# Performance work log

Measured on AMD Instinct MI355X. Metric: run time of the kernel, lower is better.

The kernel has to match this reference:

```python
import jax, jax.numpy as jnp
import numpy as np

NUM_CHUNKS = 8
TOP_K = 2
IN_FEATURES = 4096
OUT_FEATURES = 4096
BATCH = 16384
CHUNK_IN = IN_FEATURES // NUM_CHUNKS
CHUNK_OUT = OUT_FEATURES // NUM_CHUNKS


def setup_inputs() -> dict:
    key = jax.random.key(0)
    kx, kw, kb = jax.random.split(key, 3)
    x = jax.random.normal(kx, (BATCH, IN_FEATURES), dtype=jnp.float32)
    # per-chunk expert weights, stored as [num_chunks, chunk_in, chunk_out]
    W = jax.random.normal(kw, (NUM_CHUNKS, CHUNK_IN, CHUNK_OUT), dtype=jnp.float32) * (1.0 / np.sqrt(CHUNK_IN))
    b = jax.random.normal(kb, (NUM_CHUNKS, CHUNK_OUT), dtype=jnp.float32) * 0.01
    return {"x": x, "W": W, "b": b}


def reference(x, W, b):
    B = x.shape[0]
    num_chunks, chunk_in, chunk_out = W.shape
    # torch.chunk(x, num_chunks, dim=1) == reshape to [B, num_chunks, chunk_in]
    xc = x.reshape(B, num_chunks, chunk_in)
    # per-chunk mean |x| over the whole chunk tensor (batch and features)
    activities = jnp.mean(jnp.abs(xc), axis=(0, 2))  # [num_chunks]
    _, topk_indices = jax.lax.top_k(activities, TOP_K)  # descending, like torch.topk
    # gather selected chunks and their experts, one batched matmul
    xs = xc[:, topk_indices, :]                 # [B, k, chunk_in]
    ys = jnp.einsum('bki,kio->bko', xs, W[topk_indices]) + b[topk_indices]  # [B, k, chunk_out]
    output = ys.reshape(B, TOP_K * chunk_out)   # concat along dim 1 in topk order
    return output, activities, topk_indices
```

## Files before the change

### kernel.cpp

```cpp
#include <hip/hip_runtime.h>
#include <hip/hip_bf16.h>

#define BATCH     16384
#define INFEAT    4096
#define NCHUNK    8
#define CIN       512
#define COUT      512
#define ACT_GRID  2048
#define OUT_MAIN  (BATCH * 1024)
#define LDA       40

typedef short bf16x8 __attribute__((ext_vector_type(8)));
typedef float f32x4  __attribute__((ext_vector_type(4)));

static __device__ inline unsigned short f2bf_rne(float f) {
    unsigned int u = __builtin_bit_cast(unsigned int, f);
    unsigned int r = (u + 0x7fffu + ((u >> 16) & 1u)) >> 16;
    return (unsigned short)r;
}

__global__ __launch_bounds__(256, 4)
void act_partial_kernel(const float* __restrict__ x, float* __restrict__ part) {
    int t = threadIdx.x;
    float acc[4] = {0.f, 0.f, 0.f, 0.f};
    int r0 = blockIdx.x * 8;
    for (int r = 0; r < 8; ++r) {
        const float4* p = reinterpret_cast<const float4*>(x + (size_t)(r0 + r) * INFEAT);
#pragma unroll
        for (int c = 0; c < 4; ++c) {
            float4 v = p[c * 256 + t];
            acc[c] += fabsf(v.x) + fabsf(v.y) + fabsf(v.z) + fabsf(v.w);
        }
    }
#pragma unroll
    for (int c = 0; c < 4; ++c) {
        float v = acc[c];
        v += __shfl_xor(v, 32); v += __shfl_xor(v, 16); v += __shfl_xor(v, 8);
        v += __shfl_xor(v, 4);  v += __shfl_xor(v, 2);  v += __shfl_xor(v, 1);
        acc[c] = v;
    }
    __shared__ float sred[16];
    int wave = t >> 6, lane = t & 63;
    if (lane == 0) {
#pragma unroll
        for (int c = 0; c < 4; ++c) sred[wave * 4 + c] = acc[c];
    }
    __syncthreads();
    if (t < 8) {
        int c = t >> 1, hi = t & 1;
        part[t * ACT_GRID + blockIdx.x] = sred[(2 * hi) * 4 + c] + sred[(2 * hi + 1) * 4 + c];
    }
}

template <typename ShD>
static __device__ inline void topk_preamble(const float* __restrict__ part, int tt,
                                            ShD* sd, double* act8, int* sidx) {
    int ch = tt >> 5, g = tt & 31;
    double a = 0.0;
    for (int j = 0; j < 64; ++j) a += (double)part[ch * ACT_GRID + g + 32 * j];
    sd[tt] = a;
    __syncthreads();
    if (tt < 8) {
        double tot = 0.0;
        for (int j = 0; j < 32; ++j) tot += sd[tt * 32 + j];
        act8[tt] = tot;
    }
    __syncthreads();
    if (tt == 0) {
        int i0 = 0;
        for (int i = 1; i < 8; ++i) if (act8[i] > act8[i0]) i0 = i;
        int i1 = -1;
        for (int i = 0; i < 8; ++i) {
            if (i == i0) continue;
            if (i1 < 0 || act8[i] > act8[i1]) i1 = i;
        }
        sidx[0] = i0; sidx[1] = i1;
    }
    __syncthreads();
}

__global__ void wtrans_topk_kernel(const float* __restrict__ W, const float* __restrict__ part,
                                   float* __restrict__ out, unsigned short* __restrict__ WT) {
    __shared__ union { double sd[256]; float tile[32][33]; } sh;
    __shared__ double act8[8];
    __shared__ int sidx[2];
    int tx = threadIdx.x, ty = threadIdx.y;
    int tt = ty * 32 + tx;

    topk_preamble(part, tt, sh.sd, act8, sidx);

    int c = blockIdx.z;
    int id = sidx[c];
    if (blockIdx.x == 0 && blockIdx.y == 0 && c == 0) {
        if (tt < 8) out[OUT_MAIN + tt] = (float)(act8[tt] / ((double)BATCH * (double)CIN));
        if (tt == 0) {
            out[OUT_MAIN + 8] = (float)sidx[0];
            out[OUT_MAIN + 9] = (float)sidx[1];
        }
    }
    __syncthreads();

    const float* Wp = W + (size_t)id * (CIN * COUT);
    int i0 = blockIdx.x * 32, o0 = blockIdx.y * 32;
#pragma unroll
    for (int r = 0; r < 4; ++r)
        sh.tile[ty + r * 8][tx] = Wp[(size_t)(i0 + ty + r * 8) * COUT + o0 + tx];
    __syncthreads();
    unsigned short* WTp = WT + (size_t)c * (CIN * COUT);
#pragma unroll
    for (int r = 0; r < 4; ++r)
        WTp[(size_t)(o0 + ty + r * 8) * CIN + i0 + tx] = f2bf_rne(sh.tile[tx][ty + r * 8]);
}

__global__ __launch_bounds__(256, 2)
void gemm_topk_kernel(const float* __restrict__ x, const unsigned short* __restrict__ WT,
                      const float* __restrict__ bvec, const float* __restrict__ part,
                      float* __restrict__ out) {
    __shared__ union {
        double sd[256];
        struct { unsigned short As[128 * LDA]; unsigned short Bs[128 * LDA]; } g;
    } sh;
    __shared__ double act8[8];
    __shared__ int sidx[2];
    int t = threadIdx.x;

    topk_preamble(part, t, sh.sd, act8, sidx);

    int c = blockIdx.z;
    int idx = sidx[c];
    __syncthreads();

    int brow = blockIdx.x * 128, bn = blockIdx.y * 128;
    int lane = t & 63, wid = t >> 6;
    int wm = wid >> 1, wn = wid & 1;
    int lrow = lane & 15, lgrp = lane >> 4;
    f32x4 acc[4][4] = {};
    const float* xbase = x + (size_t)brow * INFEAT + idx * CIN;
    const unsigned short* wtbase = WT + (size_t)c * (CIN * COUT);
    int sa_m = t >> 3, sa_c = t & 7;
    int sb_n = t >> 1, sb_h = (t & 1) * 16;

    for (int kt = 0; kt < 16; ++kt) {
        int k0 = kt * 32;
        __syncthreads();
#pragma unroll
        for (int r = 0; r < 4; ++r) {
            int m = r * 32 + sa_m;
            float4 v = *reinterpret_cast<const float4*>(xbase + (size_t)m * INFEAT + k0 + sa_c * 4);
            ushort4 sv;
            sv.x = f2bf_rne(v.x); sv.y = f2bf_rne(v.y); sv.z = f2bf_rne(v.z); sv.w = f2bf_rne(v.w);
            *reinterpret_cast<ushort4*>(&sh.g.As[m * LDA + sa_c * 4]) = sv;
        }
        {
            const unsigned short* bsrc = wtbase + (size_t)(bn + sb_n) * CIN + k0 + sb_h;
            uint4 b0 = *reinterpret_cast<const uint4*>(bsrc);
            uint4 b1 = *reinterpret_cast<const uint4*>(bsrc + 8);
            unsigned short* bdst = &sh.g.Bs[sb_n * LDA + sb_h];
            *reinterpret_cast<uint4*>(bdst)     = b0;
            *reinterpret_cast<uint4*>(bdst + 8) = b1;
        }
        __syncthreads();
        bf16x8 af[4], bfr[4];
#pragma unroll
        for (int mi = 0; mi < 4; ++mi)
            af[mi] = *reinterpret_cast<const bf16x8*>(&sh.g.As[(wm * 64 + mi * 16 + lrow) * LDA + lgrp * 8]);
#pragma unroll
        for (int ni = 0; ni < 4; ++ni)
            bfr[ni] = *reinterpret_cast<const bf16x8*>(&sh.g.Bs[(wn * 64 + ni * 16 + lrow) * LDA + lgrp * 8]);
#pragma unroll
        for (int mi = 0; mi < 4; ++mi)
#pragma unroll
            for (int ni = 0; ni < 4; ++ni)
                acc[mi][ni] = __builtin_amdgcn_mfma_f32_16x16x32_bf16(af[mi], bfr[ni], acc[mi][ni], 0, 0, 0);
    }

    float bias[4];
#pragma unroll
    for (int ni = 0; ni < 4; ++ni)
        bias[ni] = bvec[idx * COUT + bn + wn * 64 + ni * 16 + lrow];
#pragma unroll
    for (int mi = 0; mi < 4; ++mi) {
#pragma unroll
        for (int r = 0; r < 4; ++r) {
            int row = brow + wm * 64 + mi * 16 + lgrp * 4 + r;
            float* orow = out + (size_t)row * 1024 + c * 512 + bn + wn * 64;
#pragma unroll
            for (int ni = 0; ni < 4; ++ni)
                orow[ni * 16 + lrow] = acc[mi][ni][r] + bias[ni];
        }
    }
}

extern "C" void kernel_launch(void* const* d_in, const int* in_sizes, int n_in,
                              void* d_out, int out_size, void* d_ws, size_t ws_size,
                              hipStream_t stream) {
    const float* x = (const float*)d_in[0];
    const float* W = (const float*)d_in[1];
    const float* bv = (const float*)d_in[2];
    float* out = (float*)d_out;

    float* part = (float*)d_ws;
    unsigned short* WT = (unsigned short*)((char*)d_ws + 65792);

    act_partial_kernel<<<ACT_GRID, 256, 0, stream>>>(x, part);
    wtrans_topk_kernel<<<dim3(16, 16, 2), dim3(32, 8), 0, stream>>>(W, part, out, WT);
    gemm_topk_kernel<<<dim3(BATCH / 128, COUT / 128, 2), 256, 0, stream>>>(x, WT, bv, part, out);
}
```

Measured before the change: 105.6 us.

## Fuse weight transpose into activity kernel by converting all eight chunks

Removes the separate top-k-dependent weight transpose kernel. All eight chunk weight matrices are transposed and converted to bf16 inside the same launch as the activity reduction, using extra blocks. The GEMM now indexes the converted weights by the selected chunk id and writes the activities and indices itself. This drops one kernel launch and one serial top-k preamble, at the cost of converting four times as much weight data (8 chunks instead of 2) and a larger workspace.

```diff
diff --git a/kernel.cpp b/kernel.cpp
--- a/kernel.cpp
+++ b/kernel.cpp
@@ -20,35 +20,55 @@
 }
 
 __global__ __launch_bounds__(256, 4)
-void act_partial_kernel(const float* __restrict__ x, float* __restrict__ part) {
+void act_wtrans_kernel(const float* __restrict__ x, const float* __restrict__ W,
+                       float* __restrict__ part, unsigned short* __restrict__ WT8) {
+    __shared__ union { float sred[16]; float tile[32][33]; } sh;
     int t = threadIdx.x;
-    float acc[4] = {0.f, 0.f, 0.f, 0.f};
-    int r0 = blockIdx.x * 8;
-    for (int r = 0; r < 8; ++r) {
-        const float4* p = reinterpret_cast<const float4*>(x + (size_t)(r0 + r) * INFEAT);
+    int bid = blockIdx.x;
+
+    if (bid < ACT_GRID) {
+        float acc[4] = {0.f, 0.f, 0.f, 0.f};
+        int r0 = bid * 8;
+        for (int r = 0; r < 8; ++r) {
+            const float4* p = reinterpret_cast<const float4*>(x + (size_t)(r0 + r) * INFEAT);
+#pragma unroll
+            for (int c = 0; c < 4; ++c) {
+                float4 v = p[c * 256 + t];
+                acc[c] += fabsf(v.x) + fabsf(v.y) + fabsf(v.z) + fabsf(v.w);
+            }
+        }
 #pragma unroll
         for (int c = 0; c < 4; ++c) {
-            float4 v = p[c * 256 + t];
-            acc[c] += fabsf(v.x) + fabsf(v.y) + fabsf(v.z) + fabsf(v.w);
-        }
-    }
-#pragma unroll
-    for (int c = 0; c < 4; ++c) {
-        float v = acc[c];
-        v += __shfl_xor(v, 32); v += __shfl_xor(v, 16); v += __shfl_xor(v, 8);
-        v += __shfl_xor(v, 4);  v += __shfl_xor(v, 2);  v += __shfl_xor(v, 1);
-        acc[c] = v;
-    }
-    __shared__ float sred[16];
-    int wave = t >> 6, lane = t & 63;
-    if (lane == 0) {
-#pragma unroll
-        for (int c = 0; c < 4; ++c) sred[wave * 4 + c] = acc[c];
-    }
-    __syncthreads();
-    if (t < 8) {
-        int c = t >> 1, hi = t & 1;
-        part[t * ACT_GRID + blockIdx.x] = sred[(2 * hi) * 4 + c] + sred[(2 * hi + 1) * 4 + c];
+            float v = acc[c];
+            v += __shfl_xor(v, 32); v += __shfl_xor(v, 16); v += __shfl_xor(v, 8);
+            v += __shfl_xor(v, 4);  v += __shfl_xor(v, 2);  v += __shfl_xor(v, 1);
+            acc[c] = v;
+        }
+        int wave = t >> 6, lane = t & 63;
+        if (lane == 0) {
+#pragma unroll
+            for (int c = 0; c < 4; ++c) sh.sred[wave * 4 + c] = acc[c];
+        }
+        __syncthreads();
+        if (t < 8) {
+            int c = t >> 1, hi = t & 1;
+            part[t * ACT_GRID + bid] = sh.sred[(2 * hi) * 4 + c] + sh.sred[(2 * hi + 1) * 4 + c];
+        }
+    } else {
+        int tl = bid - ACT_GRID;
+        int ch = tl >> 8;
+        int tile = tl & 255;
+        int i0 = (tile & 15) * 32, o0 = (tile >> 4) * 32;
+        int tx = t & 31, ty = t >> 5;
+        const float* Wp = W + (size_t)ch * (CIN * COUT);
+#pragma unroll
+        for (int r = 0; r < 4; ++r)
+            sh.tile[ty + r * 8][tx] = Wp[(size_t)(i0 + ty + r * 8) * COUT + o0 + tx];
+        __syncthreads();
+        unsigned short* WTp = WT8 + (size_t)ch * (CIN * COUT);
+#pragma unroll
+        for (int r = 0; r < 4; ++r)
+            WTp[(size_t)(o0 + ty + r * 8) * CIN + i0 + tx] = f2bf_rne(sh.tile[tx][ty + r * 8]);
     }
 }
 
@@ -79,41 +99,8 @@
     __syncthreads();
 }
 
-__global__ void wtrans_topk_kernel(const float* __restrict__ W, const float* __restrict__ part,
-                                   float* __restrict__ out, unsigned short* __restrict__ WT) {
-    __shared__ union { double sd[256]; float tile[32][33]; } sh;
-    __shared__ double act8[8];
-    __shared__ int sidx[2];
-    int tx = threadIdx.x, ty = threadIdx.y;
-    int tt = ty * 32 + tx;
-
-    topk_preamble(part, tt, sh.sd, act8, sidx);
-
-    int c = blockIdx.z;
-    int id = sidx[c];
-    if (blockIdx.x == 0 && blockIdx.y == 0 && c == 0) {
-        if (tt < 8) out[OUT_MAIN + tt] = (float)(act8[tt] / ((double)BATCH * (double)CIN));
-        if (tt == 0) {
-            out[OUT_MAIN + 8] = (float)sidx[0];
-            out[OUT_MAIN + 9] = (float)sidx[1];
-        }
-    }
-    __syncthreads();
-
-    const float* Wp = W + (size_t)id * (CIN * COUT);
-    int i0 = blockIdx.x * 32, o0 = blockIdx.y * 32;
-#pragma unroll
-    for (int r = 0; r < 4; ++r)
-        sh.tile[ty + r * 8][tx] = Wp[(size_t)(i0 + ty + r * 8) * COUT + o0 + tx];
-    __syncthreads();
-    unsigned short* WTp = WT + (size_t)c * (CIN * COUT);
-#pragma unroll
-    for (int r = 0; r < 4; ++r)
-        WTp[(size_t)(o0 + ty + r * 8) * CIN + i0 + tx] = f2bf_rne(sh.tile[tx][ty + r * 8]);
-}
-
 __global__ __launch_bounds__(256, 2)
-void gemm_topk_kernel(const float* __restrict__ x, const unsigned short* __restrict__ WT,
+void gemm_topk_kernel(const float* __restrict__ x, const unsigned short* __restrict__ WT8,
                       const float* __restrict__ bvec, const float* __restrict__ part,
                       float* __restrict__ out) {
     __shared__ union {
@@ -128,6 +115,13 @@
 
     int c = blockIdx.z;
     int idx = sidx[c];
+    if (blockIdx.x == 0 && blockIdx.y == 0 && c == 0) {
+        if (t < 8) out[OUT_MAIN + t] = (float)(act8[t] / ((double)BATCH * (double)CIN));
+        if (t == 0) {
+            out[OUT_MAIN + 8] = (float)sidx[0];
+            out[OUT_MAIN + 9] = (float)sidx[1];
+        }
+    }
     __syncthreads();
 
     int brow = blockIdx.x * 128, bn = blockIdx.y * 128;
@@ -136,7 +130,7 @@
     int lrow = lane & 15, lgrp = lane >> 4;
     f32x4 acc[4][4] = {};
     const float* xbase = x + (size_t)brow * INFEAT + idx * CIN;
-    const unsigned short* wtbase = WT + (size_t)c * (CIN * COUT);
+    const unsigned short* wtbase = WT8 + (size_t)idx * (CIN * COUT);
     int sa_m = t >> 3, sa_c = t & 7;
     int sb_n = t >> 1, sb_h = (t & 1) * 16;
 
@@ -200,9 +194,8 @@
     float* out = (float*)d_out;
 
     float* part = (float*)d_ws;
-    unsigned short* WT = (unsigned short*)((char*)d_ws + 65792);
-
-    act_partial_kernel<<<ACT_GRID, 256, 0, stream>>>(x, part);
-    wtrans_topk_kernel<<<dim3(16, 16, 2), dim3(32, 8), 0, stream>>>(W, part, out, WT);
-    gemm_topk_kernel<<<dim3(BATCH / 128, COUT / 128, 2), 256, 0, stream>>>(x, WT, bv, part, out);
-}
+    unsigned short* WT8 = (unsigned short*)((char*)d_ws + 65792);
+
+    act_wtrans_kernel<<<2 * ACT_GRID, 256, 0, stream>>>(x, W, part, WT8);
+    gemm_topk_kernel<<<dim3(BATCH / 128, COUT / 128, 2), 256, 0, stream>>>(x, WT8, bv, part, out);
+}
```

Measured after the change: 103.3 us. -2.2%, faster.
